# Performance work log

Hardware: AMD Instinct MI355X
Metric: run time of the kernel (lower is better)

The kernel has to match this reference:

```python
import jax, jax.numpy as jnp
import numpy as np

NUM_EXPERTS = 8
AUX_LOSS_COEF = 0.01


def setup_inputs() -> dict:
    key = jax.random.key(0)
    ks = jax.random.split(key, 5)
    B, S, D, E, H = 4, 2048, 1024, NUM_EXPERTS, 4096
    scale = 0.02  # typical init scale so gelu/softmax stay in sane ranges
    return {
        "hidden_states": jax.random.normal(ks[0], (B, S, D), dtype=jnp.float32),
        "router_w": jax.random.normal(ks[1], (D, E), dtype=jnp.float32) * scale,
        "router_b": jnp.zeros((E,), dtype=jnp.float32),
        "w1": jax.random.normal(ks[2], (E, D, H), dtype=jnp.float32) * scale,
        "b1": jnp.zeros((E, H), dtype=jnp.float32),
        "w2": jax.random.normal(ks[3], (E, H, D), dtype=jnp.float32) * scale,
        "b2": jnp.zeros((E, D), dtype=jnp.float32),
    }


def reference(hidden_states, router_w, router_b, w1, b1, w2, b2):
    B, S, D = hidden_states.shape
    E = w1.shape[0]
    x = hidden_states.reshape(-1, D)  # [T, D] flattened tokens

    # Switch router: top-1 expert, combine weight = softmax prob of chosen expert
    logits = x @ router_w + router_b                      # [T, E]
    probs = jax.nn.softmax(logits, axis=-1)               # [T, E]
    sel = jnp.argmax(logits, axis=-1)                     # [T] int
    gate = jnp.take_along_axis(probs, sel[:, None], axis=1)[:, 0]  # [T]

    # Expert FFNs: per-expert Linear -> gelu -> Linear, masked top-1 combine.
    # Loop is over the small fixed expert count (structurally distinct weights).
    out = jnp.zeros_like(x)
    for e in range(E):
        h = jax.nn.gelu(x @ w1[e] + b1[e])                # [T, H]
        ye = h @ w2[e] + b2[e]                            # [T, D]
        mask = (sel == e).astype(x.dtype)
        out = out + (mask * gate)[:, None] * ye

    # Switch load-balancing auxiliary loss
    mean_probs = probs.mean(axis=0)                       # [E]
    assignments = jnp.mean(jax.nn.one_hot(sel, E, dtype=x.dtype), axis=0)  # [E]
    aux_loss = jnp.sum(mean_probs * assignments) * E
    total_loss = AUX_LOSS_COEF * aux_loss

    return out.reshape(B, S, D), total_loss
```

## Files before the change

### kernel.cpp

```cpp
#include <hip/hip_runtime.h>
#include <cstdint>

typedef __bf16 bf16_t;
typedef __attribute__((ext_vector_type(8))) __bf16 bf16x8;
typedef __attribute__((ext_vector_type(4))) __bf16 bf16x4;
typedef __attribute__((ext_vector_type(4))) float f32x4;
typedef unsigned short ushort_t;

#define TOKENS 8192
#define DIM 1024
#define HID 4096
#define NEXP 8

__device__ __forceinline__ void gl_lds16(const void* g, void* l) {
  __builtin_amdgcn_global_load_lds(
      (__attribute__((address_space(1))) void*)(void*)g,
      (__attribute__((address_space(3))) void*)l, 16, 0, 0);
}

__device__ __forceinline__ float gelu_tanh(float x) {
  float z = 0.7978845608028654f * (x + 0.044715f * x * x * x);
  z = fminf(fmaxf(z, -15.f), 15.f);
  float e = __expf(-2.f * z);
  float th = (1.f - e) / (1.f + e);
  return 0.5f * x * (1.f + th);
}

__global__ void cvt_x_kernel(const float* __restrict__ in, bf16_t* __restrict__ out, int n4) {
  int i = blockIdx.x * blockDim.x + threadIdx.x;
  int stride = gridDim.x * blockDim.x;
  for (; i < n4; i += stride) {
    float4 v = ((const float4*)in)[i];
    bf16x4 o;
    o[0] = (bf16_t)v.x; o[1] = (bf16_t)v.y; o[2] = (bf16_t)v.z; o[3] = (bf16_t)v.w;
    ((bf16x4*)out)[i] = o;
  }
}

__global__ void tcvt_kernel(const float* __restrict__ in, bf16_t* __restrict__ out, int R, int C) {
  __shared__ float tile[64][65];
  int e = blockIdx.z;
  const float* src = in + (size_t)e * R * C;
  bf16_t* dst = out + (size_t)e * R * C;
  int rb = blockIdx.y * 64, cb = blockIdx.x * 64;
  int t = threadIdx.x;
  int r = t >> 2, cq = (t & 3) * 16;
  const float* sp = src + (size_t)(rb + r) * C + cb + cq;
#pragma unroll
  for (int j = 0; j < 16; j += 4) {
    float4 v = *(const float4*)(sp + j);
    tile[r][cq + j + 0] = v.x; tile[r][cq + j + 1] = v.y;
    tile[r][cq + j + 2] = v.z; tile[r][cq + j + 3] = v.w;
  }
  __syncthreads();
  int oc = t >> 2, orr = (t & 3) * 16;
  ushort_t tmp[16];
#pragma unroll
  for (int j = 0; j < 16; ++j) {
    bf16_t b = (bf16_t)tile[orr + j][oc];
    tmp[j] = __builtin_bit_cast(ushort_t, b);
  }
  uint4* dp = (uint4*)(dst + (size_t)(cb + oc) * R + rb + orr);
  dp[0] = ((uint4*)tmp)[0];
  dp[1] = ((uint4*)tmp)[1];
}

__global__ void router_kernel(const float* __restrict__ x, const float* __restrict__ rw,
                              const float* __restrict__ rbias, int* __restrict__ sel,
                              float* __restrict__ gate, float* __restrict__ pprob,
                              int* __restrict__ pcnt) {
  __shared__ float sprob[NEXP];
  __shared__ int scnt[NEXP];
  int t = threadIdx.x, lane = t & 63, wave = t >> 6;
  if (t < NEXP) { sprob[t] = 0.f; scnt[t] = 0; }
  __syncthreads();
  int tok = blockIdx.x * 4 + wave;
  const float* xp = x + (size_t)tok * DIM + lane * 16;
  float acc[NEXP];
#pragma unroll
  for (int e = 0; e < NEXP; ++e) acc[e] = 0.f;
#pragma unroll
  for (int j = 0; j < 16; j += 4) {
    float4 v = *(const float4*)(xp + j);
    const float* wr = rw + (size_t)(lane * 16 + j) * NEXP;
    float c[4] = {v.x, v.y, v.z, v.w};
#pragma unroll
    for (int d = 0; d < 4; ++d)
#pragma unroll
      for (int e = 0; e < NEXP; ++e) acc[e] += c[d] * wr[d * NEXP + e];
  }
#pragma unroll
  for (int s = 1; s < 64; s <<= 1)
#pragma unroll
    for (int e = 0; e < NEXP; ++e) acc[e] += __shfl_xor(acc[e], s);
  if (lane == 0) {
    float lg[NEXP];
#pragma unroll
    for (int e = 0; e < NEXP; ++e) lg[e] = acc[e] + rbias[e];
    float mx = lg[0]; int am = 0;
#pragma unroll
    for (int e = 1; e < NEXP; ++e) if (lg[e] > mx) { mx = lg[e]; am = e; }
    float p[NEXP]; float se = 0.f;
#pragma unroll
    for (int e = 0; e < NEXP; ++e) { p[e] = __expf(lg[e] - mx); se += p[e]; }
    float inv = 1.f / se;
#pragma unroll
    for (int e = 0; e < NEXP; ++e) { p[e] *= inv; atomicAdd(&sprob[e], p[e]); }
    sel[tok] = am;
    gate[tok] = p[am];
    atomicAdd(&scnt[am], 1);
  }
  __syncthreads();
  if (t < NEXP) {
    pprob[blockIdx.x * NEXP + t] = sprob[t];
    pcnt[blockIdx.x * NEXP + t] = scnt[t];
  }
}

__global__ void reduce_kernel(const float* __restrict__ pprob, const int* __restrict__ pcnt,
                              int nb, int* __restrict__ counts, int* __restrict__ offsets,
                              int* __restrict__ cursors, float* __restrict__ loss_out) {
  __shared__ float fred[256];
  __shared__ int ired[256];
  int t = threadIdx.x;
  int e = t & 7, i0 = t >> 3;
  float fs = 0.f; int is = 0;
  for (int i = i0; i < nb; i += 32) { fs += pprob[i * 8 + e]; is += pcnt[i * 8 + e]; }
  fred[t] = fs; ired[t] = is;
  __syncthreads();
  if (t < NEXP) {
    float tp = 0.f; int tc = 0;
    for (int j = 0; j < 32; ++j) { tp += fred[j * 8 + t]; tc += ired[j * 8 + t]; }
    counts[t] = tc;
    fred[t] = tp;
    cursors[t] = 0;
  }
  __syncthreads();
  if (t == 0) {
    int off = 0; float loss = 0.f;
    for (int q = 0; q < NEXP; ++q) {
      offsets[q] = off; off += counts[q];
      loss += (fred[q] / (float)TOKENS) * ((float)counts[q] / (float)TOKENS);
    }
    *loss_out = loss * (float)NEXP * 0.01f;
  }
}

__global__ void scatter_kernel(const int* __restrict__ sel, const int* __restrict__ offsets,
                               int* __restrict__ cursors, int* __restrict__ idxl) {
  int tok = blockIdx.x * 256 + threadIdx.x;
  int lane = threadIdx.x & 63;
  int e = sel[tok];
#pragma unroll
  for (int ex = 0; ex < NEXP; ++ex) {
    unsigned long long mask = __ballot(e == ex);
    if (e == ex) {
      int leader = __ffsll(mask) - 1;
      int total = __popcll(mask);
      int rank = __popcll(mask & ((1ull << lane) - 1ull));
      int base = 0;
      if (lane == leader) base = atomicAdd(&cursors[ex], total);
      base = __shfl(base, leader);
      idxl[offsets[ex] + base + rank] = tok;
    }
  }
}

__global__ __launch_bounds__(256) void gemm1_kernel(
    const bf16_t* __restrict__ xb, const bf16_t* __restrict__ w1t,
    const float* __restrict__ b1, const int* __restrict__ idxl,
    const int* __restrict__ counts, const int* __restrict__ offsets,
    bf16_t* __restrict__ h) {
  int e = blockIdx.z;
  int cnt = counts[e];
  int mBase = blockIdx.y * 128;
  if (mBase >= cnt) return;
  int nBase = blockIdx.x * 128;
  int off = offsets[e];
  __shared__ bf16_t As[4096], Bs[4096];
  int t = threadIdx.x, lane = t & 63, wave = t >> 6;
  int wrow = wave >> 1, wcol = wave & 1;
  f32x4 acc[4][4];
#pragma unroll
  for (int m = 0; m < 4; ++m)
#pragma unroll
    for (int n = 0; n < 4; ++n) acc[m][n] = (f32x4){0.f, 0.f, 0.f, 0.f};

  int srow = wave * 16 + (lane >> 2);
  int kin = (lane & 3) * 8;
  int c1 = cnt - 1;
  int slot0 = mBase + srow; slot0 = slot0 < c1 ? slot0 : c1;
  int slot1 = mBase + srow + 64; slot1 = slot1 < c1 ? slot1 : c1;
  int tok0 = idxl[off + slot0], tok1 = idxl[off + slot1];
  const bf16_t* ag0 = xb + (size_t)tok0 * DIM + kin;
  const bf16_t* ag1 = xb + (size_t)tok1 * DIM + kin;
  const bf16_t* wb = w1t + (size_t)e * HID * DIM;
  const bf16_t* bg0 = wb + (size_t)(nBase + srow) * DIM + kin;
  const bf16_t* bg1 = bg0 + (size_t)64 * DIM;
  bf16_t* lA0 = As + wave * 512;
  bf16_t* lA1 = As + 2048 + wave * 512;
  bf16_t* lB0 = Bs + wave * 512;
  bf16_t* lB1 = Bs + 2048 + wave * 512;
  int kcol = (lane >> 4) * 8;

  for (int kt = 0; kt < DIM / 32; ++kt) {
    int k0 = kt * 32;
    gl_lds16(ag0 + k0, lA0);
    gl_lds16(ag1 + k0, lA1);
    gl_lds16(bg0 + k0, lB0);
    gl_lds16(bg1 + k0, lB1);
    __syncthreads();
    bf16x8 af[4], bv[4];
#pragma unroll
    for (int m = 0; m < 4; ++m)
      af[m] = *(const bf16x8*)(As + (wrow * 64 + m * 16 + (lane & 15)) * 32 + kcol);
#pragma unroll
    for (int n = 0; n < 4; ++n)
      bv[n] = *(const bf16x8*)(Bs + (wcol * 64 + n * 16 + (lane & 15)) * 32 + kcol);
#pragma unroll
    for (int m = 0; m < 4; ++m)
#pragma unroll
      for (int n = 0; n < 4; ++n)
        acc[m][n] = __builtin_amdgcn_mfma_f32_16x16x32_bf16(af[m], bv[n], acc[m][n], 0, 0, 0);
    __syncthreads();
  }

  float bias[4];
#pragma unroll
  for (int n = 0; n < 4; ++n) bias[n] = b1[e * HID + nBase + wcol * 64 + n * 16 + (lane & 15)];
#pragma unroll
  for (int m = 0; m < 4; ++m) {
    int rb0 = mBase + wrow * 64 + m * 16 + (lane >> 4) * 4;
#pragma unroll
    for (int j = 0; j < 4; ++j) {
      int r = rb0 + j;
      if (r < cnt) {
        bf16_t* hp = h + (size_t)(off + r) * HID + nBase + wcol * 64 + (lane & 15);
#pragma unroll
        for (int n = 0; n < 4; ++n)
          hp[n * 16] = (bf16_t)gelu_tanh(acc[m][n][j] + bias[n]);
      }
    }
  }
}

__global__ __launch_bounds__(256) void gemm2_kernel(
    const bf16_t* __restrict__ h, const bf16_t* __restrict__ w2t,
    const float* __restrict__ b2, const int* __restrict__ idxl,
    const float* __restrict__ gate, const int* __restrict__ counts,
    const int* __restrict__ offsets, float* __restrict__ out) {
  int e = blockIdx.z;
  int cnt = counts[e];
  int mBase = blockIdx.y * 128;
  if (mBase >= cnt) return;
  int nBase = blockIdx.x * 128;
  int off = offsets[e];
  __shared__ bf16_t As[4096], Bs[4096];
  int t = threadIdx.x, lane = t & 63, wave = t >> 6;
  int wrow = wave >> 1, wcol = wave & 1;
  f32x4 acc[4][4];
#pragma unroll
  for (int m = 0; m < 4; ++m)
#pragma unroll
    for (int n = 0; n < 4; ++n) acc[m][n] = (f32x4){0.f, 0.f, 0.f, 0.f};

  int srow = wave * 16 + (lane >> 2);
  int kin = (lane & 3) * 8;
  const bf16_t* ag0 = h + (size_t)(off + mBase + srow) * HID + kin;
  const bf16_t* ag1 = ag0 + (size_t)64 * HID;
  const bf16_t* wb = w2t + (size_t)e * DIM * HID;
  const bf16_t* bg0 = wb + (size_t)(nBase + srow) * HID + kin;
  const bf16_t* bg1 = bg0 + (size_t)64 * HID;
  bf16_t* lA0 = As + wave * 512;
  bf16_t* lA1 = As + 2048 + wave * 512;
  bf16_t* lB0 = Bs + wave * 512;
  bf16_t* lB1 = Bs + 2048 + wave * 512;
  int kcol = (lane >> 4) * 8;

  for (int kt = 0; kt < HID / 32; ++kt) {
    int k0 = kt * 32;
    gl_lds16(ag0 + k0, lA0);
    gl_lds16(ag1 + k0, lA1);
    gl_lds16(bg0 + k0, lB0);
    gl_lds16(bg1 + k0, lB1);
    __syncthreads();
    bf16x8 af[4], bv[4];
#pragma unroll
    for (int m = 0; m < 4; ++m)
      af[m] = *(const bf16x8*)(As + (wrow * 64 + m * 16 + (lane & 15)) * 32 + kcol);
#pragma unroll
    for (int n = 0; n < 4; ++n)
      bv[n] = *(const bf16x8*)(Bs + (wcol * 64 + n * 16 + (lane & 15)) * 32 + kcol);
#pragma unroll
    for (int m = 0; m < 4; ++m)
#pragma unroll
      for (int n = 0; n < 4; ++n)
        acc[m][n] = __builtin_amdgcn_mfma_f32_16x16x32_bf16(af[m], bv[n], acc[m][n], 0, 0, 0);
    __syncthreads();
  }

  float bias[4];
#pragma unroll
  for (int n = 0; n < 4; ++n) bias[n] = b2[e * DIM + nBase + wcol * 64 + n * 16 + (lane & 15)];
#pragma unroll
  for (int m = 0; m < 4; ++m) {
    int rb0 = mBase + wrow * 64 + m * 16 + (lane >> 4) * 4;
#pragma unroll
    for (int j = 0; j < 4; ++j) {
      int r = rb0 + j;
      if (r < cnt) {
        int tok = idxl[off + r];
        float g = gate[tok];
        float* op = out + (size_t)tok * DIM + nBase + wcol * 64 + (lane & 15);
#pragma unroll
        for (int n = 0; n < 4; ++n)
          op[n * 16] = g * (acc[m][n][j] + bias[n]);
      }
    }
  }
}

extern "C" void kernel_launch(void* const* d_in, const int* in_sizes, int n_in,
                              void* d_out, int out_size, void* d_ws, size_t ws_size,
                              hipStream_t stream) {
  const float* hs = (const float*)d_in[0];
  const float* rw = (const float*)d_in[1];
  const float* rb = (const float*)d_in[2];
  const float* w1 = (const float*)d_in[3];
  const float* b1 = (const float*)d_in[4];
  const float* w2 = (const float*)d_in[5];
  const float* b2 = (const float*)d_in[6];
  float* out = (float*)d_out;
  char* ws = (char*)d_ws;

  bf16_t* xb   = (bf16_t*)(ws + 0);
  bf16_t* w1t  = (bf16_t*)(ws + 16777216);
  bf16_t* w2t  = (bf16_t*)(ws + 83886080);
  bf16_t* hbuf = (bf16_t*)(ws + 150994944);
  int*   sel   = (int*)  (ws + 219152384);
  float* gate  = (float*)(ws + 219185152);
  int*   idxl  = (int*)  (ws + 219217920);
  float* pprob = (float*)(ws + 219250688);
  int*   pcnt  = (int*)  (ws + 219316224);
  int*   counts  = (int*)(ws + 219381760);
  int*   offsets = counts + 8;
  int*   cursors = counts + 16;

  cvt_x_kernel<<<2048, 256, 0, stream>>>(hs, xb, TOKENS * DIM / 4);
  tcvt_kernel<<<dim3(64, 16, 8), 256, 0, stream>>>(w1, w1t, DIM, HID);
  tcvt_kernel<<<dim3(16, 64, 8), 256, 0, stream>>>(w2, w2t, HID, DIM);
  router_kernel<<<2048, 256, 0, stream>>>(hs, rw, rb, sel, gate, pprob, pcnt);
  reduce_kernel<<<1, 256, 0, stream>>>(pprob, pcnt, 2048, counts, offsets, cursors,
                                       out + (out_size - 1));
  scatter_kernel<<<32, 256, 0, stream>>>(sel, offsets, cursors, idxl);
  gemm1_kernel<<<dim3(32, 64, 8), 256, 0, stream>>>(xb, w1t, b1, idxl, counts, offsets, hbuf);
  gemm2_kernel<<<dim3(8, 64, 8), 256, 0, stream>>>(hbuf, w2t, b2, idxl, gate, counts, offsets, out);
}
```

Baseline: 409.4 us.

## Fuse x conversion into router, merge weight transposes, shrink gemm2 M tile

The router kernel now also writes the bf16 copy of the activations, which removes the separate conversion kernel and a second full read of the input. The two weight transpose-convert launches are merged into one kernel launch. gemm2 moves from 128-row to 64-row M tiles with a combined shared buffer and clamped row indices, which doubles the grid to improve occupancy and load balance on the per-expert N=1024 GEMM. In exchange, B-tile reuse per block is lower and each block issues more MFMA loads per output.

Result: slower. 434.9 us (+6.2%).

```diff
diff --git a/kernel.cpp b/kernel.cpp
--- a/kernel.cpp
+++ b/kernel.cpp
@@ -3,7 +3,6 @@
 
 typedef __bf16 bf16_t;
 typedef __attribute__((ext_vector_type(8))) __bf16 bf16x8;
-typedef __attribute__((ext_vector_type(4))) __bf16 bf16x4;
 typedef __attribute__((ext_vector_type(4))) float f32x4;
 typedef unsigned short ushort_t;
 
@@ -26,23 +25,78 @@
   return 0.5f * x * (1.f + th);
 }
 
-__global__ void cvt_x_kernel(const float* __restrict__ in, bf16_t* __restrict__ out, int n4) {
-  int i = blockIdx.x * blockDim.x + threadIdx.x;
-  int stride = gridDim.x * blockDim.x;
-  for (; i < n4; i += stride) {
-    float4 v = ((const float4*)in)[i];
-    bf16x4 o;
-    o[0] = (bf16_t)v.x; o[1] = (bf16_t)v.y; o[2] = (bf16_t)v.z; o[3] = (bf16_t)v.w;
-    ((bf16x4*)out)[i] = o;
-  }
-}
-
-__global__ void tcvt_kernel(const float* __restrict__ in, bf16_t* __restrict__ out, int R, int C) {
+__global__ void router_kernel(const float* __restrict__ x, const float* __restrict__ rw,
+                              const float* __restrict__ rbias, bf16_t* __restrict__ xb,
+                              int* __restrict__ sel, float* __restrict__ gate,
+                              float* __restrict__ pprob, int* __restrict__ pcnt) {
+  __shared__ float sprob[NEXP];
+  __shared__ int scnt[NEXP];
+  int t = threadIdx.x, lane = t & 63, wave = t >> 6;
+  if (t < NEXP) { sprob[t] = 0.f; scnt[t] = 0; }
+  __syncthreads();
+  int tok = blockIdx.x * 4 + wave;
+  const float* xp = x + (size_t)tok * DIM + lane * 16;
+  float acc[NEXP];
+#pragma unroll
+  for (int e = 0; e < NEXP; ++e) acc[e] = 0.f;
+  ushort_t xv[16];
+#pragma unroll
+  for (int j = 0; j < 16; j += 4) {
+    float4 v = *(const float4*)(xp + j);
+    const float* wr = rw + (size_t)(lane * 16 + j) * NEXP;
+    float c[4] = {v.x, v.y, v.z, v.w};
+#pragma unroll
+    for (int d = 0; d < 4; ++d) {
+      xv[j + d] = __builtin_bit_cast(ushort_t, (bf16_t)c[d]);
+#pragma unroll
+      for (int e = 0; e < NEXP; ++e) acc[e] += c[d] * wr[d * NEXP + e];
+    }
+  }
+  {
+    uint4* xop = (uint4*)(xb + (size_t)tok * DIM + lane * 16);
+    xop[0] = ((uint4*)xv)[0];
+    xop[1] = ((uint4*)xv)[1];
+  }
+#pragma unroll
+  for (int s = 1; s < 64; s <<= 1)
+#pragma unroll
+    for (int e = 0; e < NEXP; ++e) acc[e] += __shfl_xor(acc[e], s);
+  if (lane == 0) {
+    float lg[NEXP];
+#pragma unroll
+    for (int e = 0; e < NEXP; ++e) lg[e] = acc[e] + rbias[e];
+    float mx = lg[0]; int am = 0;
+#pragma unroll
+    for (int e = 1; e < NEXP; ++e) if (lg[e] > mx) { mx = lg[e]; am = e; }
+    float p[NEXP]; float se = 0.f;
+#pragma unroll
+    for (int e = 0; e < NEXP; ++e) { p[e] = __expf(lg[e] - mx); se += p[e]; }
+    float inv = 1.f / se;
+#pragma unroll
+    for (int e = 0; e < NEXP; ++e) { p[e] *= inv; atomicAdd(&sprob[e], p[e]); }
+    sel[tok] = am;
+    gate[tok] = p[am];
+    atomicAdd(&scnt[am], 1);
+  }
+  __syncthreads();
+  if (t < NEXP) {
+    pprob[blockIdx.x * NEXP + t] = sprob[t];
+    pcnt[blockIdx.x * NEXP + t] = scnt[t];
+  }
+}
+
+__global__ void tcvt2_kernel(const float* __restrict__ w1, const float* __restrict__ w2,
+                             bf16_t* __restrict__ w1t, bf16_t* __restrict__ w2t) {
   __shared__ float tile[64][65];
-  int e = blockIdx.z;
-  const float* src = in + (size_t)e * R * C;
-  bf16_t* dst = out + (size_t)e * R * C;
-  int rb = blockIdx.y * 64, cb = blockIdx.x * 64;
+  int y = blockIdx.y;
+  int which = y >> 3, e = y & 7;
+  int R = which ? HID : DIM;
+  int C = which ? DIM : HID;
+  const float* src = (which ? w2 : w1) + (size_t)e * R * C;
+  bf16_t* dst = (which ? w2t : w1t) + (size_t)e * R * C;
+  int cbt = C >> 6;
+  int rt = blockIdx.x / cbt, ct = blockIdx.x % cbt;
+  int rb = rt * 64, cb = ct * 64;
   int t = threadIdx.x;
   int r = t >> 2, cq = (t & 3) * 16;
   const float* sp = src + (size_t)(rb + r) * C + cb + cq;
@@ -63,58 +117,6 @@
   uint4* dp = (uint4*)(dst + (size_t)(cb + oc) * R + rb + orr);
   dp[0] = ((uint4*)tmp)[0];
   dp[1] = ((uint4*)tmp)[1];
-}
-
-__global__ void router_kernel(const float* __restrict__ x, const float* __restrict__ rw,
-                              const float* __restrict__ rbias, int* __restrict__ sel,
-                              float* __restrict__ gate, float* __restrict__ pprob,
-                              int* __restrict__ pcnt) {
-  __shared__ float sprob[NEXP];
-  __shared__ int scnt[NEXP];
-  int t = threadIdx.x, lane = t & 63, wave = t >> 6;
-  if (t < NEXP) { sprob[t] = 0.f; scnt[t] = 0; }
-  __syncthreads();
-  int tok = blockIdx.x * 4 + wave;
-  const float* xp = x + (size_t)tok * DIM + lane * 16;
-  float acc[NEXP];
-#pragma unroll
-  for (int e = 0; e < NEXP; ++e) acc[e] = 0.f;
-#pragma unroll
-  for (int j = 0; j < 16; j += 4) {
-    float4 v = *(const float4*)(xp + j);
-    const float* wr = rw + (size_t)(lane * 16 + j) * NEXP;
-    float c[4] = {v.x, v.y, v.z, v.w};
-#pragma unroll
-    for (int d = 0; d < 4; ++d)
-#pragma unroll
-      for (int e = 0; e < NEXP; ++e) acc[e] += c[d] * wr[d * NEXP + e];
-  }
-#pragma unroll
-  for (int s = 1; s < 64; s <<= 1)
-#pragma unroll
-    for (int e = 0; e < NEXP; ++e) acc[e] += __shfl_xor(acc[e], s);
-  if (lane == 0) {
-    float lg[NEXP];
-#pragma unroll
-    for (int e = 0; e < NEXP; ++e) lg[e] = acc[e] + rbias[e];
-    float mx = lg[0]; int am = 0;
-#pragma unroll
-    for (int e = 1; e < NEXP; ++e) if (lg[e] > mx) { mx = lg[e]; am = e; }
-    float p[NEXP]; float se = 0.f;
-#pragma unroll
-    for (int e = 0; e < NEXP; ++e) { p[e] = __expf(lg[e] - mx); se += p[e]; }
-    float inv = 1.f / se;
-#pragma unroll
-    for (int e = 0; e < NEXP; ++e) { p[e] *= inv; atomicAdd(&sprob[e], p[e]); }
-    sel[tok] = am;
-    gate[tok] = p[am];
-    atomicAdd(&scnt[am], 1);
-  }
-  __syncthreads();
-  if (t < NEXP) {
-    pprob[blockIdx.x * NEXP + t] = sprob[t];
-    pcnt[blockIdx.x * NEXP + t] = scnt[t];
-  }
 }
 
 __global__ void reduce_kernel(const float* __restrict__ pprob, const int* __restrict__ pcnt,
@@ -251,48 +253,54 @@
     const int* __restrict__ offsets, float* __restrict__ out) {
   int e = blockIdx.z;
   int cnt = counts[e];
-  int mBase = blockIdx.y * 128;
+  int mBase = blockIdx.y * 64;
   if (mBase >= cnt) return;
   int nBase = blockIdx.x * 128;
   int off = offsets[e];
-  __shared__ bf16_t As[4096], Bs[4096];
+  __shared__ bf16_t S[6144];
   int t = threadIdx.x, lane = t & 63, wave = t >> 6;
   int wrow = wave >> 1, wcol = wave & 1;
-  f32x4 acc[4][4];
-#pragma unroll
-  for (int m = 0; m < 4; ++m)
+  f32x4 acc[2][4];
+#pragma unroll
+  for (int m = 0; m < 2; ++m)
 #pragma unroll
     for (int n = 0; n < 4; ++n) acc[m][n] = (f32x4){0.f, 0.f, 0.f, 0.f};
 
-  int srow = wave * 16 + (lane >> 2);
+  int c1 = cnt - 1;
   int kin = (lane & 3) * 8;
-  const bf16_t* ag0 = h + (size_t)(off + mBase + srow) * HID + kin;
-  const bf16_t* ag1 = ag0 + (size_t)64 * HID;
-  const bf16_t* wb = w2t + (size_t)e * DIM * HID;
-  const bf16_t* bg0 = wb + (size_t)(nBase + srow) * HID + kin;
-  const bf16_t* bg1 = bg0 + (size_t)64 * HID;
-  bf16_t* lA0 = As + wave * 512;
-  bf16_t* lA1 = As + 2048 + wave * 512;
-  bf16_t* lB0 = Bs + wave * 512;
-  bf16_t* lB1 = Bs + 2048 + wave * 512;
+  const bf16_t* srcp[3];
+  bf16_t* ldst[3];
+#pragma unroll
+  for (int i = 0; i < 3; ++i) {
+    int c = wave * 3 + i;
+    int row = c * 16 + (lane >> 2);
+    const bf16_t* p;
+    if (row < 64) {
+      int slot = mBase + row; slot = slot < c1 ? slot : c1;
+      p = h + (size_t)(off + slot) * HID + kin;
+    } else {
+      p = w2t + (size_t)e * DIM * HID + (size_t)(nBase + row - 64) * HID + kin;
+    }
+    srcp[i] = p;
+    ldst[i] = S + c * 512;
+  }
   int kcol = (lane >> 4) * 8;
 
   for (int kt = 0; kt < HID / 32; ++kt) {
     int k0 = kt * 32;
-    gl_lds16(ag0 + k0, lA0);
-    gl_lds16(ag1 + k0, lA1);
-    gl_lds16(bg0 + k0, lB0);
-    gl_lds16(bg1 + k0, lB1);
+    gl_lds16(srcp[0] + k0, ldst[0]);
+    gl_lds16(srcp[1] + k0, ldst[1]);
+    gl_lds16(srcp[2] + k0, ldst[2]);
     __syncthreads();
-    bf16x8 af[4], bv[4];
-#pragma unroll
-    for (int m = 0; m < 4; ++m)
-      af[m] = *(const bf16x8*)(As + (wrow * 64 + m * 16 + (lane & 15)) * 32 + kcol);
+    bf16x8 af[2], bv[4];
+#pragma unroll
+    for (int m = 0; m < 2; ++m)
+      af[m] = *(const bf16x8*)(S + (wrow * 32 + m * 16 + (lane & 15)) * 32 + kcol);
 #pragma unroll
     for (int n = 0; n < 4; ++n)
-      bv[n] = *(const bf16x8*)(Bs + (wcol * 64 + n * 16 + (lane & 15)) * 32 + kcol);
-#pragma unroll
-    for (int m = 0; m < 4; ++m)
+      bv[n] = *(const bf16x8*)(S + 2048 + (wcol * 64 + n * 16 + (lane & 15)) * 32 + kcol);
+#pragma unroll
+    for (int m = 0; m < 2; ++m)
 #pragma unroll
       for (int n = 0; n < 4; ++n)
         acc[m][n] = __builtin_amdgcn_mfma_f32_16x16x32_bf16(af[m], bv[n], acc[m][n], 0, 0, 0);
@@ -303,8 +311,8 @@
 #pragma unroll
   for (int n = 0; n < 4; ++n) bias[n] = b2[e * DIM + nBase + wcol * 64 + n * 16 + (lane & 15)];
 #pragma unroll
-  for (int m = 0; m < 4; ++m) {
-    int rb0 = mBase + wrow * 64 + m * 16 + (lane >> 4) * 4;
+  for (int m = 0; m < 2; ++m) {
+    int rb0 = mBase + wrow * 32 + m * 16 + (lane >> 4) * 4;
 #pragma unroll
     for (int j = 0; j < 4; ++j) {
       int r = rb0 + j;
@@ -346,13 +354,11 @@
   int*   offsets = counts + 8;
   int*   cursors = counts + 16;
 
-  cvt_x_kernel<<<2048, 256, 0, stream>>>(hs, xb, TOKENS * DIM / 4);
-  tcvt_kernel<<<dim3(64, 16, 8), 256, 0, stream>>>(w1, w1t, DIM, HID);
-  tcvt_kernel<<<dim3(16, 64, 8), 256, 0, stream>>>(w2, w2t, HID, DIM);
-  router_kernel<<<2048, 256, 0, stream>>>(hs, rw, rb, sel, gate, pprob, pcnt);
+  router_kernel<<<2048, 256, 0, stream>>>(hs, rw, rb, xb, sel, gate, pprob, pcnt);
+  tcvt2_kernel<<<dim3(1024, 16), 256, 0, stream>>>(w1, w2, w1t, w2t);
   reduce_kernel<<<1, 256, 0, stream>>>(pprob, pcnt, 2048, counts, offsets, cursors,
                                        out + (out_size - 1));
   scatter_kernel<<<32, 256, 0, stream>>>(sel, offsets, cursors, idxl);
   gemm1_kernel<<<dim3(32, 64, 8), 256, 0, stream>>>(xb, w1t, b1, idxl, counts, offsets, hbuf);
-  gemm2_kernel<<<dim3(8, 64, 8), 256, 0, stream>>>(hbuf, w2t, b2, idxl, gate, counts, offsets, out);
-}
+  gemm2_kernel<<<dim3(8, 128, 8), 256, 0, stream>>>(hbuf, w2t, b2, idxl, gate, counts, offsets, out);
+}
```
